# Optimization experiments

Measured on AMD Instinct MI355X. Metric: run time of the kernel, lower is better.

## Reference

```python
import jax, jax.numpy as jnp
import numpy as np
from jax import lax

STRIDE = (1, 1)
PADDING = ((1, 1), (1, 1))
DILATION = (1, 1)


def setup_inputs() -> dict:
    key = jax.random.key(0)
    k1, k2, k3, k4 = jax.random.split(key, 4)
    bs, cin, h, w = 64, 128, 56, 56
    k_exp, cout, kh, kw = 8, 128, 3, 3
    x = jax.random.normal(k1, (bs, cin, h, w), dtype=jnp.float32)
    routing_weight = jax.random.uniform(k2, (bs, k_exp), dtype=jnp.float32)
    weight = jax.random.normal(k3, (k_exp, cout, cin, kh, kw), dtype=jnp.float32) * (1.0 / np.sqrt(cin * kh * kw))
    bias = jax.random.normal(k4, (k_exp, cout), dtype=jnp.float32) * 0.01
    return {"x": x, "routing_weight": routing_weight, "weight": weight, "bias": bias}


def reference(x, routing_weight, weight, bias):
    # CondConv combine_kernel path: per-sample kernel = routing-weighted sum of experts,
    # then a standard conv per sample (equivalent to torch groups=bs trick).
    # w_mix: [bs, oc, c, kh, kw]
    w_mix = jnp.einsum('bk,kocij->bocij', routing_weight, weight)
    b_mix = routing_weight @ bias  # [bs, oc]

    def conv_one(xi, wi):
        # xi: [c, h, w], wi: [oc, c, kh, kw]
        return lax.conv_general_dilated(
            xi[None], wi,
            window_strides=STRIDE,
            padding=PADDING,
            rhs_dilation=DILATION,
            dimension_numbers=('NCHW', 'OIHW', 'NCHW'),
        )[0]  # [oc, oh, ow]

    out = jax.vmap(conv_one)(x, w_mix)  # [bs, oc, oh, ow]
    out = out + b_mix[:, :, None, None]
    return out
```

## Files before the change

### kernel.cpp

```cpp
#include <hip/hip_runtime.h>

#define BS    64
#define CIN   128
#define OCH   128
#define HW    56
#define KEXP  8
#define KTOT  1152
#define NSTEP 36
#define PLANEC 3364
#define WMIX_PS (NSTEP * OCH * 32)
#define TPAD  58

typedef __bf16 bf16x8 __attribute__((ext_vector_type(8)));
typedef float  f32x4  __attribute__((ext_vector_type(4)));

__device__ __forceinline__ unsigned f2bf(float f) {
    union { float f; unsigned u; } v; v.f = f;
    unsigned r = v.u + 0x7fffu + ((v.u >> 16) & 1u);
    return r >> 16;
}

__device__ __forceinline__ void gl16(const unsigned short* g, unsigned short* l) {
    __builtin_amdgcn_global_load_lds(
        (const __attribute__((address_space(1))) void*)g,
        (__attribute__((address_space(3))) void*)l, 16, 0, 0);
}

__global__ __launch_bounds__(256) void prep_xt(const float* __restrict__ x,
                                               unsigned short* __restrict__ xt) {
    __shared__ unsigned short t[CIN * TPAD];
    int b = blockIdx.x, ihp = blockIdx.y;
    int tid = threadIdx.x;
    bool border = (ihp == 0) || (ihp == 57);
    if (!border) {
        int ih = ihp - 1;
        const float* xr = x + (size_t)b * CIN * HW * HW + (size_t)ih * HW;
        #pragma unroll
        for (int i7 = 0; i7 < 7; ++i7) {
            int i = i7 * 256 + tid;
            int c = i / 14, w4 = i - c * 14;
            float4 v = *(const float4*)(xr + (size_t)c * (HW * HW) + w4 * 4);
            unsigned lo = f2bf(v.x) | (f2bf(v.y) << 16);
            unsigned hi = f2bf(v.z) | (f2bf(v.w) << 16);
            *(unsigned*)&t[c * TPAD + w4 * 4]     = lo;
            *(unsigned*)&t[c * TPAD + w4 * 4 + 2] = hi;
        }
    }
    __syncthreads();
    for (int j = tid; j < 928; j += 256) {
        int qq = j / 232, rr = j - qq * 232;
        int oct = rr / 58, col = rr - oct * 58;
        union { unsigned short u[8]; uint4 v; } o;
        o.v = make_uint4(0u, 0u, 0u, 0u);
        if (!border && col >= 1 && col <= 56) {
            #pragma unroll
            for (int k = 0; k < 8; ++k)
                o.u[k] = t[(qq * 32 + oct * 8 + k) * TPAD + (col - 1)];
        }
        *(uint4*)&xt[(((size_t)(b * 16 + qq * 4 + oct)) * PLANEC
                      + (size_t)ihp * 58 + col) * 8] = o.v;
    }
}

__global__ __launch_bounds__(256) void prep_wmix(
        const float* __restrict__ rw, const float* __restrict__ wgt,
        unsigned short* __restrict__ wmix) {
    __shared__ float wlds[KEXP * KTOT];
    __shared__ float rwl[16 * KEXP];
    int oc  = blockIdx.x;
    int bg  = blockIdx.y;
    int tid = threadIdx.x;

    if (tid < 16 * KEXP) rwl[tid] = rw[bg * 16 * KEXP + tid];
    const float* wsrc = wgt + (size_t)oc * KTOT;
    #pragma unroll
    for (int e = 0; e < KEXP; ++e) {
        const float* we = wsrc + (size_t)e * OCH * KTOT;
        for (int j = tid; j < KTOT; j += 256) wlds[e * KTOT + j] = we[j];
    }
    __syncthreads();

    for (int t = tid; t < KTOT; t += 256) {
        int c = t & 127, rs = t >> 7;
        int q = c >> 5, cl = c & 31;
        size_t oidx = ((size_t)(q * 9 + rs) * OCH + oc) * 32 + cl;
        float w8[KEXP];
        #pragma unroll
        for (int e = 0; e < KEXP; ++e) w8[e] = wlds[e * KTOT + c * 9 + rs];
        #pragma unroll
        for (int b = 0; b < 16; ++b) {
            float a = 0.f;
            #pragma unroll
            for (int e = 0; e < KEXP; ++e) a += rwl[b * KEXP + e] * w8[e];
            wmix[(size_t)(bg * 16 + b) * WMIX_PS + oidx] = (unsigned short)f2bf(a);
        }
    }
}

__global__ __launch_bounds__(256) void prep_bmix(
        const float* __restrict__ rw, const float* __restrict__ bias,
        float* __restrict__ bmix) {
    int i = blockIdx.x * 256 + threadIdx.x;
    int b = i >> 7, oc = i & 127;
    float a = 0.f;
    #pragma unroll
    for (int e = 0; e < KEXP; ++e) a += rw[b * KEXP + e] * bias[e * OCH + oc];
    bmix[i] = a;
}

__global__ __launch_bounds__(256, 4) void condconv_mfma(
        const unsigned short* __restrict__ xt, const unsigned short* __restrict__ wmix,
        const float* __restrict__ bmix, float* __restrict__ out) {
    __shared__ unsigned short patch[2][8192];

    int blk  = blockIdx.x;
    int b    = blk & 63;
    int tile = blk >> 6;
    int oh0  = tile * 2;
    int tid  = threadIdx.x;
    int wave = tid >> 6, lane = tid & 63, ln = lane & 15, quad = lane >> 4;

    const unsigned short* ap = wmix + (size_t)b * WMIX_PS
                             + (size_t)(wave * 32 + ln) * 32 + quad * 8;

    const unsigned short* xb = xt + (size_t)(b * 16) * (PLANEC * 8)
                             + (size_t)oh0 * 58 * 8;

    int rcl[4];
    #pragma unroll
    for (int i = 0; i < 4; ++i) {
        int rc = i * 64 + lane;
        rcl[i] = (rc > 231) ? 231 : rc;
    }

    int cb[7], offn[7];
    #pragma unroll
    for (int nt = 0; nt < 7; ++nt) {
        int n   = nt * 16 + ln;
        int row = (n >= 56) ? 1 : 0;
        int ow  = n - row * 56;
        cb[nt]   = (quad * 256 + row * 58 + ow) * 8;
        offn[nt] = (oh0 + row) * HW + ow;
    }

    f32x4 acc[2][7] = {};

    auto stage = [&](int qq, int bf) {
        const unsigned short* sq = xb + (size_t)(qq * 4 + wave) * (PLANEC * 8);
        #pragma unroll
        for (int i = 0; i < 4; ++i)
            gl16(sq + (size_t)rcl[i] * 8, &patch[bf][(wave * 256 + i * 64) * 8]);
    };

    stage(0, 0);
    bf16x8 pa0[2], pa1[2];
    pa0[0] = *(const bf16x8*)(ap);
    pa1[0] = *(const bf16x8*)(ap + 512);
    pa0[1] = *(const bf16x8*)(ap + 4096);
    pa1[1] = *(const bf16x8*)(ap + 4096 + 512);
    __syncthreads();

    #pragma unroll
    for (int qq = 0; qq < 4; ++qq) {
        if (qq < 3) stage(qq + 1, (qq + 1) & 1);
        #pragma unroll
        for (int s9 = 0; s9 < 9; ++s9) {
            const int s = qq * 9 + s9;
            bf16x8 ca0 = pa0[s & 1], ca1 = pa1[s & 1];
            const int sp = (s + 2 < NSTEP) ? (s + 2) : (NSTEP - 1);
            pa0[s & 1] = *(const bf16x8*)(ap + (size_t)sp * 4096);
            pa1[s & 1] = *(const bf16x8*)(ap + (size_t)sp * 4096 + 512);
            const int r = s9 / 3, sc = s9 - r * 3;
            const int pshift = (r * 58 + sc) * 8;
            #pragma unroll
            for (int nt = 0; nt < 7; ++nt) {
                bf16x8 bb = *(const bf16x8*)&patch[qq & 1][cb[nt] + pshift];
                acc[0][nt] = __builtin_amdgcn_mfma_f32_16x16x32_bf16(ca0, bb, acc[0][nt], 0, 0, 0);
                acc[1][nt] = __builtin_amdgcn_mfma_f32_16x16x32_bf16(ca1, bb, acc[1][nt], 0, 0, 0);
            }
        }
        __syncthreads();
    }

    const float* bmb = bmix + b * OCH;
    float* ob = out + (size_t)b * OCH * HW * HW;
    #pragma unroll
    for (int mt = 0; mt < 2; ++mt) {
        #pragma unroll
        for (int rg = 0; rg < 4; ++rg) {
            int oc = wave * 32 + mt * 16 + quad * 4 + rg;
            float bv = bmb[oc];
            #pragma unroll
            for (int nt = 0; nt < 7; ++nt)
                ob[(size_t)oc * (HW * HW) + offn[nt]] = acc[mt][nt][rg] + bv;
        }
    }
}

extern "C" void kernel_launch(void* const* d_in, const int* in_sizes, int n_in,
                              void* d_out, int out_size, void* d_ws, size_t ws_size,
                              hipStream_t stream) {
    (void)in_sizes; (void)n_in; (void)out_size; (void)ws_size;
    const float* x    = (const float*)d_in[0];
    const float* rw   = (const float*)d_in[1];
    const float* wgt  = (const float*)d_in[2];
    const float* bias = (const float*)d_in[3];
    float* outp = (float*)d_out;

    unsigned short* wmix = (unsigned short*)d_ws;
    float* bmix = (float*)((char*)d_ws + (size_t)BS * WMIX_PS * 2);
    unsigned short* xtw = (unsigned short*)((char*)d_ws + (size_t)BS * WMIX_PS * 2 + 32768);

    hipLaunchKernelGGL(prep_xt,   dim3(BS, 58), dim3(256), 0, stream, x, xtw);
    hipLaunchKernelGGL(prep_wmix, dim3(OCH, 4), dim3(256), 0, stream, rw, wgt, wmix);
    hipLaunchKernelGGL(prep_bmix, dim3(32),     dim3(256), 0, stream, rw, bias, bmix);
    hipLaunchKernelGGL(condconv_mfma, dim3(BS * 28), dim3(256), 0, stream,
                       xtw, wmix, bmix, outp);
}
```

Baseline: 268.2 us.

## Use two waves of 64 output channels each in conv kernel, fuse bias mix

```diff
diff --git a/kernel.cpp b/kernel.cpp
--- a/kernel.cpp
+++ b/kernel.cpp
@@ -9,9 +9,10 @@
 #define NSTEP 36
 #define PLANEC 3364
 #define WMIX_PS (NSTEP * OCH * 32)
-#define TPAD  58
+#define TPAD  60
 
 typedef __bf16 bf16x8 __attribute__((ext_vector_type(8)));
+typedef __bf16 bf16x4 __attribute__((ext_vector_type(4)));
 typedef float  f32x4  __attribute__((ext_vector_type(4)));
 
 __device__ __forceinline__ unsigned f2bf(float f) {
@@ -40,10 +41,8 @@
             int i = i7 * 256 + tid;
             int c = i / 14, w4 = i - c * 14;
             float4 v = *(const float4*)(xr + (size_t)c * (HW * HW) + w4 * 4);
-            unsigned lo = f2bf(v.x) | (f2bf(v.y) << 16);
-            unsigned hi = f2bf(v.z) | (f2bf(v.w) << 16);
-            *(unsigned*)&t[c * TPAD + w4 * 4]     = lo;
-            *(unsigned*)&t[c * TPAD + w4 * 4 + 2] = hi;
+            bf16x4 pk = { (__bf16)v.x, (__bf16)v.y, (__bf16)v.z, (__bf16)v.w };
+            *(bf16x4*)&t[c * TPAD + w4 * 4] = pk;
         }
     }
     __syncthreads();
@@ -64,7 +63,8 @@
 
 __global__ __launch_bounds__(256) void prep_wmix(
         const float* __restrict__ rw, const float* __restrict__ wgt,
-        unsigned short* __restrict__ wmix) {
+        const float* __restrict__ bias,
+        unsigned short* __restrict__ wmix, float* __restrict__ bmix) {
     __shared__ float wlds[KEXP * KTOT];
     __shared__ float rwl[16 * KEXP];
     int oc  = blockIdx.x;
@@ -80,6 +80,13 @@
     }
     __syncthreads();
 
+    if (tid < 16) {
+        float a = 0.f;
+        #pragma unroll
+        for (int e = 0; e < KEXP; ++e) a += rwl[tid * KEXP + e] * bias[e * OCH + oc];
+        bmix[(size_t)(bg * 16 + tid) * OCH + oc] = a;
+    }
+
     for (int t = tid; t < KTOT; t += 256) {
         int c = t & 127, rs = t >> 7;
         int q = c >> 5, cl = c & 31;
@@ -97,18 +104,7 @@
     }
 }
 
-__global__ __launch_bounds__(256) void prep_bmix(
-        const float* __restrict__ rw, const float* __restrict__ bias,
-        float* __restrict__ bmix) {
-    int i = blockIdx.x * 256 + threadIdx.x;
-    int b = i >> 7, oc = i & 127;
-    float a = 0.f;
-    #pragma unroll
-    for (int e = 0; e < KEXP; ++e) a += rw[b * KEXP + e] * bias[e * OCH + oc];
-    bmix[i] = a;
-}
-
-__global__ __launch_bounds__(256, 4) void condconv_mfma(
+__global__ __launch_bounds__(128, 2) void condconv_mfma(
         const unsigned short* __restrict__ xt, const unsigned short* __restrict__ wmix,
         const float* __restrict__ bmix, float* __restrict__ out) {
     __shared__ unsigned short patch[2][8192];
@@ -121,16 +117,17 @@
     int wave = tid >> 6, lane = tid & 63, ln = lane & 15, quad = lane >> 4;
 
     const unsigned short* ap = wmix + (size_t)b * WMIX_PS
-                             + (size_t)(wave * 32 + ln) * 32 + quad * 8;
+                             + (size_t)(wave * 64 + ln) * 32 + quad * 8;
 
     const unsigned short* xb = xt + (size_t)(b * 16) * (PLANEC * 8)
                              + (size_t)oh0 * 58 * 8;
 
-    int rcl[4];
-    #pragma unroll
-    for (int i = 0; i < 4; ++i) {
-        int rc = i * 64 + lane;
-        rcl[i] = (rc > 231) ? 231 : rc;
+    int rcl[8], octl[8];
+    #pragma unroll
+    for (int i = 0; i < 8; ++i) {
+        int rc = (i & 3) * 64 + lane;
+        rcl[i]  = (rc > 231) ? 231 : rc;
+        octl[i] = 2 * wave + (i >> 2);
     }
 
     int cb[7], offn[7];
@@ -143,21 +140,24 @@
         offn[nt] = (oh0 + row) * HW + ow;
     }
 
-    f32x4 acc[2][7] = {};
+    f32x4 acc[4][7] = {};
 
     auto stage = [&](int qq, int bf) {
-        const unsigned short* sq = xb + (size_t)(qq * 4 + wave) * (PLANEC * 8);
-        #pragma unroll
-        for (int i = 0; i < 4; ++i)
-            gl16(sq + (size_t)rcl[i] * 8, &patch[bf][(wave * 256 + i * 64) * 8]);
+        #pragma unroll
+        for (int i = 0; i < 8; ++i) {
+            const unsigned short* src = xb
+                + ((size_t)(qq * 4 + octl[i]) * PLANEC + rcl[i]) * 8;
+            gl16(src, &patch[bf][wave * 4096 + i * 512]);
+        }
     };
 
     stage(0, 0);
-    bf16x8 pa0[2], pa1[2];
-    pa0[0] = *(const bf16x8*)(ap);
-    pa1[0] = *(const bf16x8*)(ap + 512);
-    pa0[1] = *(const bf16x8*)(ap + 4096);
-    pa1[1] = *(const bf16x8*)(ap + 4096 + 512);
+    bf16x8 pa[2][4];
+    #pragma unroll
+    for (int mt = 0; mt < 4; ++mt) {
+        pa[0][mt] = *(const bf16x8*)(ap + mt * 512);
+        pa[1][mt] = *(const bf16x8*)(ap + 4096 + mt * 512);
+    }
     __syncthreads();
 
     #pragma unroll
@@ -166,17 +166,22 @@
         #pragma unroll
         for (int s9 = 0; s9 < 9; ++s9) {
             const int s = qq * 9 + s9;
-            bf16x8 ca0 = pa0[s & 1], ca1 = pa1[s & 1];
+            bf16x8 ca[4];
+            #pragma unroll
+            for (int mt = 0; mt < 4; ++mt) ca[mt] = pa[s & 1][mt];
             const int sp = (s + 2 < NSTEP) ? (s + 2) : (NSTEP - 1);
-            pa0[s & 1] = *(const bf16x8*)(ap + (size_t)sp * 4096);
-            pa1[s & 1] = *(const bf16x8*)(ap + (size_t)sp * 4096 + 512);
+            #pragma unroll
+            for (int mt = 0; mt < 4; ++mt)
+                pa[s & 1][mt] = *(const bf16x8*)(ap + (size_t)sp * 4096 + mt * 512);
             const int r = s9 / 3, sc = s9 - r * 3;
             const int pshift = (r * 58 + sc) * 8;
             #pragma unroll
             for (int nt = 0; nt < 7; ++nt) {
                 bf16x8 bb = *(const bf16x8*)&patch[qq & 1][cb[nt] + pshift];
-                acc[0][nt] = __builtin_amdgcn_mfma_f32_16x16x32_bf16(ca0, bb, acc[0][nt], 0, 0, 0);
-                acc[1][nt] = __builtin_amdgcn_mfma_f32_16x16x32_bf16(ca1, bb, acc[1][nt], 0, 0, 0);
+                acc[0][nt] = __builtin_amdgcn_mfma_f32_16x16x32_bf16(ca[0], bb, acc[0][nt], 0, 0, 0);
+                acc[1][nt] = __builtin_amdgcn_mfma_f32_16x16x32_bf16(ca[1], bb, acc[1][nt], 0, 0, 0);
+                acc[2][nt] = __builtin_amdgcn_mfma_f32_16x16x32_bf16(ca[2], bb, acc[2][nt], 0, 0, 0);
+                acc[3][nt] = __builtin_amdgcn_mfma_f32_16x16x32_bf16(ca[3], bb, acc[3][nt], 0, 0, 0);
             }
         }
         __syncthreads();
@@ -185,10 +190,10 @@
     const float* bmb = bmix + b * OCH;
     float* ob = out + (size_t)b * OCH * HW * HW;
     #pragma unroll
-    for (int mt = 0; mt < 2; ++mt) {
+    for (int mt = 0; mt < 4; ++mt) {
         #pragma unroll
         for (int rg = 0; rg < 4; ++rg) {
-            int oc = wave * 32 + mt * 16 + quad * 4 + rg;
+            int oc = wave * 64 + mt * 16 + quad * 4 + rg;
             float bv = bmb[oc];
             #pragma unroll
             for (int nt = 0; nt < 7; ++nt)
@@ -212,8 +217,7 @@
     unsigned short* xtw = (unsigned short*)((char*)d_ws + (size_t)BS * WMIX_PS * 2 + 32768);
 
     hipLaunchKernelGGL(prep_xt,   dim3(BS, 58), dim3(256), 0, stream, x, xtw);
-    hipLaunchKernelGGL(prep_wmix, dim3(OCH, 4), dim3(256), 0, stream, rw, wgt, wmix);
-    hipLaunchKernelGGL(prep_bmix, dim3(32),     dim3(256), 0, stream, rw, bias, bmix);
-    hipLaunchKernelGGL(condconv_mfma, dim3(BS * 28), dim3(256), 0, stream,
+    hipLaunchKernelGGL(prep_wmix, dim3(OCH, 4), dim3(256), 0, stream, rw, wgt, bias, wmix, bmix);
+    hipLaunchKernelGGL(condconv_mfma, dim3(BS * 28), dim3(128), 0, stream,
                        xtw, wmix, bmix, outp);
 }
```

Result: slower. 274.9 us (+2.5%).
